# Kernel optimization log

Hardware: AMD Instinct MI355X
Metric: run time of the kernel (lower is better)

## Reference

```python
import jax, jax.numpy as jnp
import numpy as np

T, N, E = 12, 20000, 320000
FIN, H, G, C = 128, 256, 256, 10


def setup_inputs() -> dict:
    key = jax.random.key(0)
    ks = jax.random.split(key, 14)
    x = jax.random.normal(ks[0], (T, N, FIN), dtype=jnp.float32)
    edge_index = jax.random.randint(ks[1], (T, 2, E), 0, N)
    edge_attr = jax.random.uniform(ks[2], (T, E), dtype=jnp.float32)

    def lin(k, fan_in, shape):
        return jax.random.normal(k, shape, dtype=jnp.float32) / np.sqrt(fan_in).astype(np.float32)

    return {
        "x": x,
        "edge_index": edge_index,
        "edge_attr": edge_attr,
        "W1": lin(ks[3], FIN, (FIN, H)),
        "b1": jnp.zeros((H,), jnp.float32),
        "W2": lin(ks[4], H, (H, H)),
        "b2": jnp.zeros((H,), jnp.float32),
        "Wih": lin(ks[5], H, (3 * G, H)),
        "Whh": lin(ks[6], G, (3 * G, G)),
        "bih": jnp.zeros((3 * G,), jnp.float32),
        "bhh": jnp.zeros((3 * G,), jnp.float32),
        "Wc": lin(ks[7], G, (G, C)),
        "bc": jnp.zeros((C,), jnp.float32),
    }


def _gcn_conv(h, row, col, w, W, b):
    # PyG GCNConv: h' = D^{-1/2} (A + I) D^{-1/2} (h W) + b, with edge weights w
    h = h @ W  # [N, H]
    deg = jax.ops.segment_sum(w, col, num_segments=N) + 1.0  # self-loop weight 1
    dinv = jax.lax.rsqrt(deg)  # [N]
    norm = dinv[row] * w * dinv[col]  # [E]
    agg = jax.ops.segment_sum(norm[:, None] * h[row], col, num_segments=N)
    agg = agg + (dinv * dinv)[:, None] * h  # self-loop contribution
    return agg + b


def reference(x, edge_index, edge_attr, W1, b1, W2, b2, Wih, Whh, bih, bhh, Wc, bc):
    def snapshot(carry, inp):
        xs, ei, ea = inp
        row, col = ei[0], ei[1]
        h = jax.nn.relu(_gcn_conv(xs, row, col, ea, W1, b1))
        h = jax.nn.relu(_gcn_conv(h, row, col, ea, W2, b2))
        return carry, h.mean(axis=0)  # mean pool over nodes -> [H]

    _, embs = jax.lax.scan(snapshot, 0, (x, edge_index, edge_attr))  # [T, H]

    def gru_step(hprev, xt):
        gx = Wih @ xt + bih  # [3G]
        gh = Whh @ hprev + bhh
        r = jax.nn.sigmoid(gx[:G] + gh[:G])
        z = jax.nn.sigmoid(gx[G:2 * G] + gh[G:2 * G])
        n = jnp.tanh(gx[2 * G:] + r * gh[2 * G:])
        hnew = (1.0 - z) * n + z * hprev
        return hnew, None

    last_h, _ = jax.lax.scan(gru_step, jnp.zeros((G,), x.dtype), embs)
    out = last_h @ Wc + bc  # [C]
    return out[None, :]  # [1, num_classes]
```

## Files before the change

kernel.cpp:

```cpp
#include <hip/hip_runtime.h>
#include <hip/hip_fp16.h>
#include <math.h>

#define T_ 12
#define N_ 20000
#define E_ 320000
#define FIN_ 128
#define H_ 256
#define G_ 256
#define C_ 10
#define ECH 8
#define EPC (E_ / ECH)
#define NB 20
#define BNODES 1024
#define CAPF 18432

typedef __attribute__((ext_vector_type(8))) short bf16x8;
typedef __attribute__((ext_vector_type(4))) float f32x4;

static const size_t OFF_EMB   = 0;
static const size_t ZERO_BYTES= 12288;
static const size_t OFF_DINV  = 12288;
static const size_t OFF_CP    = 972288;
static const size_t OFF_DEGP  = 1932544;
static const size_t OFF_CNT16 = 9612544;
static const size_t OFF_EBIN  = 1932544;
static const size_t OFF_PCNT  = 32652544;
static const size_t OFF_POFF  = 32660224;
static const size_t OFF_EREC  = 32668288;
static const size_t OFF_W1BT  = 48028288;
static const size_t OFF_W2BT  = 48093824;
static const size_t OFF_WIHT  = 48224896;
static const size_t OFF_WHHT  = 49011328;
static const size_t OFF_GX    = 49797760;
static const size_t OFF_RA    = 49834624;
static const size_t PER_T_FULL= 10240000;

__device__ __forceinline__ float bf2f(unsigned short u) {
  return __uint_as_float(((unsigned int)u) << 16);
}
__device__ __forceinline__ unsigned short f2bf(float f) {
  unsigned int u = __float_as_uint(f);
  unsigned int r = (u + 0x7FFFu + ((u >> 16) & 1u)) >> 16;
  return (unsigned short)r;
}
__device__ __forceinline__ float bflo(unsigned int u) { return __uint_as_float(u << 16); }
__device__ __forceinline__ float bfhi(unsigned int u) { return __uint_as_float(u & 0xFFFF0000u); }
__device__ __forceinline__ unsigned int packbf(float lo, float hi) {
  return (unsigned int)f2bf(lo) | ((unsigned int)f2bf(hi) << 16);
}
__device__ __forceinline__ float rec2nm(unsigned int rec) {
  return __half2float(__ushort_as_half((unsigned short)(rec >> 16)));
}

__global__ __launch_bounds__(1024) void histp(const int* __restrict__ ei,
                                              const float* __restrict__ ea,
                                              float* __restrict__ degp,
                                              unsigned short* __restrict__ cnt16) {
  __shared__ float degs[N_];
  __shared__ unsigned int cntp[N_ / 2];
  const int t = blockIdx.x, ech = blockIdx.y;
  const int tid = threadIdx.x;
  for (int i = tid; i < N_; i += 1024) degs[i] = 0.f;
  for (int i = tid; i < N_ / 2; i += 1024) cntp[i] = 0u;
  __syncthreads();
  const int* col = ei + (size_t)t * 2 * E_ + E_ + ech * EPC;
  const float* wt = ea + (size_t)t * E_ + ech * EPC;
  for (int e = tid; e < EPC; e += 1024) {
    int c = col[e];
    atomicAdd(&degs[c], wt[e]);
    atomicAdd(&cntp[c >> 1], 1u << ((c & 1) * 16));
  }
  __syncthreads();
  float* dp = degp + ((size_t)t * ECH + ech) * N_;
  unsigned short* cp16 = cnt16 + ((size_t)t * ECH + ech) * N_;
  for (int i = tid; i < N_; i += 1024) {
    dp[i] = degs[i];
    cp16[i] = (unsigned short)((cntp[i >> 1] >> ((i & 1) * 16)) & 0xFFFFu);
  }
}

__global__ __launch_bounds__(1024) void scanT(const unsigned short* __restrict__ cnt16,
                                              const float* __restrict__ degp,
                                              int* __restrict__ colptr,
                                              float* __restrict__ dinv) {
  const int t = blockIdx.x;
  __shared__ int s[1024];
  const int tid = threadIdx.x;
  int base = 0;
  for (int c0 = 0; c0 < N_; c0 += 1024) {
    int n = c0 + tid;
    int tot = 0;
    float dg = 0.f;
    if (n < N_) {
#pragma unroll
      for (int ch = 0; ch < ECH; ++ch) {
        tot += cnt16[((size_t)t * ECH + ch) * N_ + n];
        dg += degp[((size_t)t * ECH + ch) * N_ + n];
      }
    }
    s[tid] = tot;
    __syncthreads();
    for (int off = 1; off < 1024; off <<= 1) {
      int add = (tid >= off) ? s[tid - off] : 0;
      __syncthreads();
      s[tid] += add;
      __syncthreads();
    }
    if (n < N_) {
      colptr[t * (N_ + 1) + n] = base + s[tid] - tot;
      dinv[t * N_ + n] = rsqrtf(dg + 1.0f);
    }
    base += s[1023];
    __syncthreads();
  }
  if (tid == 0) colptr[t * (N_ + 1) + N_] = base;
}

__global__ __launch_bounds__(256) void pcount(const unsigned short* __restrict__ cnt16,
                                              unsigned int* __restrict__ pcnt) {
  __shared__ unsigned int psum[NB];
  const int t = blockIdx.x, ech = blockIdx.y;
  const int tid = threadIdx.x;
  if (tid < NB) psum[tid] = 0u;
  __syncthreads();
  const unsigned short* cc = cnt16 + ((size_t)t * ECH + ech) * N_;
  for (int c0 = 0; c0 < N_; c0 += 256) {
    int n = c0 + tid;
    unsigned int v = (n < N_) ? (unsigned int)cc[n] : 0u;
#pragma unroll
    for (int off = 32; off; off >>= 1) v += __shfl_down(v, off, 64);
    if ((tid & 63) == 0) atomicAdd(&psum[c0 >> 10], v);
  }
  __syncthreads();
  if (tid < NB) pcnt[((size_t)t * ECH + ech) * NB + tid] = psum[tid];
}

__global__ void partS(const unsigned int* __restrict__ pcnt,
                      unsigned int* __restrict__ poff) {
  const int t = threadIdx.x;
  if (t >= T_) return;
  unsigned int run = 0;
  for (int b = 0; b < NB; ++b)
    for (int ech = 0; ech < ECH; ++ech) {
      poff[t * 168 + b * 8 + ech] = run;
      run += pcnt[((size_t)t * ECH + ech) * NB + b];
    }
  poff[t * 168 + 160] = run;
}

__global__ __launch_bounds__(512) void partW(const int* __restrict__ ei,
                                             const float* __restrict__ ea,
                                             const float* __restrict__ dinv,
                                             const unsigned int* __restrict__ poff,
                                             uint2* __restrict__ ebin) {
  __shared__ unsigned int cursor[NB];
  const int t = blockIdx.x, ech = blockIdx.y;
  const int tid = threadIdx.x;
  if (tid < NB) cursor[tid] = poff[t * 168 + tid * 8 + ech];
  __syncthreads();
  const int eoff = ech * EPC;
  const int* rowp = ei + (size_t)t * 2 * E_ + eoff;
  const int* colp = rowp + E_;
  const float* wt = ea + (size_t)t * E_ + eoff;
  const float* dv = dinv + (size_t)t * N_;
  uint2* eb = ebin + (size_t)t * E_;
  for (int e = tid; e < EPC; e += 512) {
    int c = colp[e], r = rowp[e];
    float nm = dv[r] * wt[e] * dv[c];
    unsigned int pos = atomicAdd(&cursor[c >> 10], 1u);
    uint2 rec;
    rec.x = (unsigned int)(c & 1023) | ((unsigned int)r << 16);
    rec.y = (unsigned int)__half_as_ushort(__float2half(nm));
    eb[pos] = rec;
  }
}

__global__ __launch_bounds__(512) void fillB2(const uint2* __restrict__ ebin,
                                              const int* __restrict__ colptr,
                                              unsigned int* __restrict__ erec) {
  __shared__ unsigned int data[CAPF];
  __shared__ unsigned int offp[BNODES];
  const int t = blockIdx.x, b = blockIdx.y;
  const int tid = threadIdx.x;
  const int nlo = b << 10;
  const int nnodes = (N_ - nlo < BNODES) ? (N_ - nlo) : BNODES;
  const int* cp = colptr + t * (N_ + 1);
  const int base = cp[nlo];
  const int bsize = cp[nlo + nnodes] - base;
  for (int i = tid; i < nnodes; i += 512) offp[i] = (unsigned int)(cp[nlo + i] - base);
  __syncthreads();
  const uint2* eb = ebin + (size_t)t * E_ + base;
  unsigned int* eg = erec + (size_t)t * E_ + base;
  for (int i = tid; i < bsize; i += 512) {
    uint2 rec = eb[i];
    unsigned int cl = rec.x & 0xFFFFu;
    unsigned int rec4 = (rec.x >> 16) | (rec.y << 16);
    unsigned int pos = atomicAdd(&offp[cl], 1u);
    if (pos < CAPF) data[pos] = rec4;
    else eg[pos] = rec4;
  }
  __syncthreads();
  const int lim = bsize < CAPF ? bsize : CAPF;
  for (int i = tid; i < lim; i += 512) eg[i] = data[i];
}

__global__ __launch_bounds__(256) void prep_kernel(const float* __restrict__ W1,
                                                   const float* __restrict__ W2,
                                                   const float* __restrict__ Wih,
                                                   const float* __restrict__ Whh,
                                                   unsigned short* __restrict__ W1bT,
                                                   unsigned short* __restrict__ W2bT,
                                                   float* __restrict__ WihT,
                                                   float* __restrict__ WhhT) {
  int idx = blockIdx.x * 256 + threadIdx.x;
  if (idx < 32768) {
    int n = idx >> 7, k = idx & 127;
    W1bT[idx] = f2bf(W1[k * 256 + n]);
  } else if (idx < 98304) {
    int j = idx - 32768;
    int n = j >> 8, k = j & 255;
    W2bT[j] = f2bf(W2[k * 256 + n]);
  } else if (idx < 294912) {
    int j = idx - 98304;
    int k = j / 768, c = j - k * 768;
    WihT[j] = Wih[c * 256 + k];
  } else if (idx < 491520) {
    int j = idx - 294912;
    int k = j / 768, c = j - k * 768;
    WhhT[j] = Whh[c * 256 + k];
  }
}

__global__ __launch_bounds__(256) void castx_kernel(const float* __restrict__ x,
                                                    unsigned short* __restrict__ xb,
                                                    int t_base) {
  const int tl = blockIdx.y;
  const int t = t_base + tl;
  const size_t q = (size_t)blockIdx.x * 256 + threadIdx.x;
  float4 v = ((const float4*)x)[(size_t)t * (N_ * FIN_ / 4) + q];
  ushort4 o;
  o.x = f2bf(v.x); o.y = f2bf(v.y); o.z = f2bf(v.z); o.w = f2bf(v.w);
  ((ushort4*)xb)[(size_t)tl * (N_ * FIN_ / 4) + q] = o;
}

__device__ __forceinline__ void agg_decode(int nt, int t_base, int& t, int& tl, int& node) {
  int bid = blockIdx.x;
  int L = bid;
  if (nt > 1) {
    int chunk = (int)(gridDim.x >> 3);
    L = (bid & 7) * chunk + (bid >> 3);
  }
  tl = L / 5000;
  node = (L - tl * 5000) * 4 + ((int)threadIdx.x >> 6);
  t = t_base + tl;
}

__global__ __launch_bounds__(256) void agg128(const unsigned short* __restrict__ h,
                                              unsigned short* __restrict__ o,
                                              const unsigned int* __restrict__ erec,
                                              const int* __restrict__ colptr,
                                              const float* __restrict__ dinv,
                                              int t_base, int nt) {
  int t, tl, node;
  agg_decode(nt, t_base, t, tl, node);
  const int q = ((int)threadIdx.x >> 4) & 3;
  const int l16 = threadIdx.x & 15;
  const int me = threadIdx.x & 63;
  const unsigned int* ert = erec + (size_t)t * E_;
  const int* cp = colptr + t * (N_ + 1);
  const unsigned short* ht = h + (size_t)tl * N_ * 128;
  float a0 = 0.f, a1 = 0.f, a2 = 0.f, a3 = 0.f, a4 = 0.f, a5 = 0.f, a6 = 0.f, a7 = 0.f;
  const int s0 = cp[node], s1 = cp[node + 1];
  for (int i = s0 + q; i < s1; i += 4) {
    const unsigned int rec = ert[i];
    const int r = rec & 0xFFFFu;
    const float nm = rec2nm(rec);
    uint4 u = *(const uint4*)&ht[(size_t)r * 128 + l16 * 8];
    a0 = fmaf(nm, bflo(u.x), a0); a1 = fmaf(nm, bfhi(u.x), a1);
    a2 = fmaf(nm, bflo(u.y), a2); a3 = fmaf(nm, bfhi(u.y), a3);
    a4 = fmaf(nm, bflo(u.z), a4); a5 = fmaf(nm, bfhi(u.z), a5);
    a6 = fmaf(nm, bflo(u.w), a6); a7 = fmaf(nm, bfhi(u.w), a7);
  }
  if (q == 0) {
    const float di = dinv[(size_t)t * N_ + node];
    const float sw = di * di;
    uint4 us = *(const uint4*)&ht[(size_t)node * 128 + l16 * 8];
    a0 = fmaf(sw, bflo(us.x), a0); a1 = fmaf(sw, bfhi(us.x), a1);
    a2 = fmaf(sw, bflo(us.y), a2); a3 = fmaf(sw, bfhi(us.y), a3);
    a4 = fmaf(sw, bflo(us.z), a4); a5 = fmaf(sw, bfhi(us.z), a5);
    a6 = fmaf(sw, bflo(us.w), a6); a7 = fmaf(sw, bfhi(us.w), a7);
  }
  a0 += __shfl(a0, me | 16, 64); a1 += __shfl(a1, me | 16, 64);
  a2 += __shfl(a2, me | 16, 64); a3 += __shfl(a3, me | 16, 64);
  a4 += __shfl(a4, me | 16, 64); a5 += __shfl(a5, me | 16, 64);
  a6 += __shfl(a6, me | 16, 64); a7 += __shfl(a7, me | 16, 64);
  a0 += __shfl(a0, me | 32, 64); a1 += __shfl(a1, me | 32, 64);
  a2 += __shfl(a2, me | 32, 64); a3 += __shfl(a3, me | 32, 64);
  a4 += __shfl(a4, me | 32, 64); a5 += __shfl(a5, me | 32, 64);
  a6 += __shfl(a6, me | 32, 64); a7 += __shfl(a7, me | 32, 64);
  if (q == 0 && (me >> 4) == 0) {
    uint4 ov;
    ov.x = packbf(a0, a1); ov.y = packbf(a2, a3);
    ov.z = packbf(a4, a5); ov.w = packbf(a6, a7);
    *(uint4*)&o[((size_t)tl * N_ + node) * 128 + l16 * 8] = ov;
  }
}

__global__ __launch_bounds__(256) void agg256(const unsigned short* __restrict__ h,
                                              unsigned short* __restrict__ o,
                                              const unsigned int* __restrict__ erec,
                                              const int* __restrict__ colptr,
                                              const float* __restrict__ dinv,
                                              int t_base, int nt) {
  int t, tl, node;
  agg_decode(nt, t_base, t, tl, node);
  const int hh = ((int)threadIdx.x >> 5) & 1;
  const int l32 = threadIdx.x & 31;
  const int me = threadIdx.x & 63;
  const unsigned int* ert = erec + (size_t)t * E_;
  const int* cp = colptr + t * (N_ + 1);
  const unsigned short* ht = h + (size_t)tl * N_ * 256;
  float a0 = 0.f, a1 = 0.f, a2 = 0.f, a3 = 0.f, a4 = 0.f, a5 = 0.f, a6 = 0.f, a7 = 0.f;
  const int s0 = cp[node], s1 = cp[node + 1];
  for (int i = s0 + hh; i < s1; i += 2) {
    const unsigned int rec = ert[i];
    const int r = rec & 0xFFFFu;
    const float nm = rec2nm(rec);
    uint4 u = *(const uint4*)&ht[(size_t)r * 256 + l32 * 8];
    a0 = fmaf(nm, bflo(u.x), a0); a1 = fmaf(nm, bfhi(u.x), a1);
    a2 = fmaf(nm, bflo(u.y), a2); a3 = fmaf(nm, bfhi(u.y), a3);
    a4 = fmaf(nm, bflo(u.z), a4); a5 = fmaf(nm, bfhi(u.z), a5);
    a6 = fmaf(nm, bflo(u.w), a6); a7 = fmaf(nm, bfhi(u.w), a7);
  }
  if (hh == 0) {
    const float di = dinv[(size_t)t * N_ + node];
    const float sw = di * di;
    uint4 us = *(const uint4*)&ht[(size_t)node * 256 + l32 * 8];
    a0 = fmaf(sw, bflo(us.x), a0); a1 = fmaf(sw, bfhi(us.x), a1);
    a2 = fmaf(sw, bflo(us.y), a2); a3 = fmaf(sw, bfhi(us.y), a3);
    a4 = fmaf(sw, bflo(us.z), a4); a5 = fmaf(sw, bfhi(us.z), a5);
    a6 = fmaf(sw, bflo(us.w), a6); a7 = fmaf(sw, bfhi(us.w), a7);
  }
  a0 += __shfl(a0, me | 32, 64); a1 += __shfl(a1, me | 32, 64);
  a2 += __shfl(a2, me | 32, 64); a3 += __shfl(a3, me | 32, 64);
  a4 += __shfl(a4, me | 32, 64); a5 += __shfl(a5, me | 32, 64);
  a6 += __shfl(a6, me | 32, 64); a7 += __shfl(a7, me | 32, 64);
  if (hh == 0) {
    uint4 ov;
    ov.x = packbf(a0, a1); ov.y = packbf(a2, a3);
    ov.z = packbf(a4, a5); ov.w = packbf(a6, a7);
    *(uint4*)&o[((size_t)tl * N_ + node) * 256 + l32 * 8] = ov;
  }
}

template <int K, bool MEAN>
__global__ __launch_bounds__(256) void gemm_bf16(const unsigned short* __restrict__ A,
                                                 const unsigned short* __restrict__ BT,
                                                 const float* __restrict__ bias,
                                                 unsigned short* __restrict__ C,
                                                 float* __restrict__ embp,
                                                 int t_base) {
  constexpr int LD = K + 8;
  __shared__ unsigned short As[64 * LD];
  __shared__ float cs[128];
  const int tid = threadIdx.x;
  const int tl = blockIdx.z;
  const int bm = blockIdx.x * 64;
  const int bn = blockIdx.y * 128;
  const unsigned short* At = A + (size_t)tl * N_ * K;
  if (MEAN && tid < 128) cs[tid] = 0.f;
  {
    constexpr int CPR = K / 8;
    constexpr int CH = 64 * CPR / 256;
#pragma unroll
    for (int i = 0; i < CH; ++i) {
      int chunk = tid + i * 256;
      int r = chunk / CPR;
      int ck = (chunk - r * CPR) * 8;
      int row = bm + r;
      if (row >= N_) row = N_ - 1;
      *(bf16x8*)&As[r * LD + ck] = *(const bf16x8*)&At[(size_t)row * K + ck];
    }
  }
  __syncthreads();
  const int w = tid >> 6, l = tid & 63;
  const int l16 = l & 15, lk = l >> 4;
  const int rbase = (w >> 1) * 32;
  const int colbase = bn + (w & 1) * 64;
  f32x4 acc[2][4] = {};
  for (int ks = 0; ks < K; ks += 32) {
    bf16x8 a[2], b[4];
#pragma unroll
    for (int m = 0; m < 2; ++m)
      a[m] = *(const bf16x8*)&As[(rbase + m * 16 + l16) * LD + ks + lk * 8];
#pragma unroll
    for (int n = 0; n < 4; ++n)
      b[n] = *(const bf16x8*)&BT[(size_t)(colbase + n * 16 + l16) * K + ks + lk * 8];
#pragma unroll
    for (int m = 0; m < 2; ++m)
#pragma unroll
      for (int n = 0; n < 4; ++n)
        acc[m][n] = __builtin_amdgcn_mfma_f32_16x16x32_bf16(a[m], b[n], acc[m][n], 0, 0, 0);
  }
#pragma unroll
  for (int n = 0; n < 4; ++n) {
    int col = colbase + n * 16 + l16;
    float bv = bias[col];
    float psum = 0.f;
#pragma unroll
    for (int m = 0; m < 2; ++m) {
      int row0 = bm + rbase + m * 16 + lk * 4;
#pragma unroll
      for (int r = 0; r < 4; ++r) {
        int row = row0 + r;
        if (row < N_) {
          float v = fmaxf(acc[m][n][r] + bv, 0.f);
          if (MEAN) psum += v;
          else C[((size_t)tl * N_ + row) * 256 + col] = f2bf(v);
        }
      }
    }
    if (MEAN) atomicAdd(&cs[col - bn], psum);
  }
  if (MEAN) {
    __syncthreads();
    if (tid < 128)
      atomicAdd(&embp[(t_base + tl) * 256 + bn + tid], cs[tid] * (1.0f / N_));
  }
}

__global__ __launch_bounds__(768) void gx_kernel(const float* __restrict__ emb,
                                                 const float* __restrict__ WihT,
                                                 const float* __restrict__ bih,
                                                 float* __restrict__ GX) {
  const int t = blockIdx.x;
  const int tid = threadIdx.x;
  __shared__ float se[256];
  if (tid < 256) se[tid] = emb[t * 256 + tid];
  __syncthreads();
  float p0 = 0.f, p1 = 0.f, p2 = 0.f, p3 = 0.f;
#pragma unroll 8
  for (int k = 0; k < 256; k += 4) {
    p0 = fmaf(WihT[(size_t)(k + 0) * 768 + tid], se[k + 0], p0);
    p1 = fmaf(WihT[(size_t)(k + 1) * 768 + tid], se[k + 1], p1);
    p2 = fmaf(WihT[(size_t)(k + 2) * 768 + tid], se[k + 2], p2);
    p3 = fmaf(WihT[(size_t)(k + 3) * 768 + tid], se[k + 3], p3);
  }
  GX[t * 768 + tid] = (p0 + p1) + (p2 + p3) + bih[tid];
}

__global__ __launch_bounds__(768) void gru2_kernel(const float* __restrict__ GX,
                                                   const float* __restrict__ WhhT,
                                                   const float* __restrict__ bhh,
                                                   const float* __restrict__ Wc,
                                                   const float* __restrict__ bc,
                                                   float* __restrict__ out) {
  __shared__ float sh[256];
  __shared__ float sgh[768];
  const int tid = threadIdx.x;
  if (tid < 256) sh[tid] = 0.f;
  __syncthreads();
  for (int t = 0; t < T_; ++t) {
    float p0 = 0.f, p1 = 0.f, p2 = 0.f, p3 = 0.f;
#pragma unroll 8
    for (int k = 0; k < 256; k += 4) {
      p0 = fmaf(WhhT[(size_t)(k + 0) * 768 + tid], sh[k + 0], p0);
      p1 = fmaf(WhhT[(size_t)(k + 1) * 768 + tid], sh[k + 1], p1);
      p2 = fmaf(WhhT[(size_t)(k + 2) * 768 + tid], sh[k + 2], p2);
      p3 = fmaf(WhhT[(size_t)(k + 3) * 768 + tid], sh[k + 3], p3);
    }
    sgh[tid] = (p0 + p1) + (p2 + p3) + bhh[tid];
    __syncthreads();
    if (tid < 256) {
      const float* gx = &GX[t * 768];
      float r = 1.f / (1.f + __expf(-(gx[tid] + sgh[tid])));
      float z = 1.f / (1.f + __expf(-(gx[256 + tid] + sgh[256 + tid])));
      float n = tanhf(gx[512 + tid] + r * sgh[512 + tid]);
      sh[tid] = (1.f - z) * n + z * sh[tid];
    }
    __syncthreads();
  }
  const int wv = tid >> 6, lane = tid & 63;
  if (wv < C_) {
    float p = 0.f;
#pragma unroll
    for (int i = 0; i < 4; ++i) {
      int j = lane + 64 * i;
      p += sh[j] * Wc[(size_t)j * C_ + wv];
    }
    for (int off = 32; off > 0; off >>= 1) p += __shfl_down(p, off);
    if (lane == 0) out[wv] = p + bc[wv];
  }
}

extern "C" void kernel_launch(void* const* d_in, const int* in_sizes, int n_in,
                              void* d_out, int out_size, void* d_ws, size_t ws_size,
                              hipStream_t stream) {
  const float* x   = (const float*)d_in[0];
  const int*   ei  = (const int*)d_in[1];
  const float* ea  = (const float*)d_in[2];
  const float* W1  = (const float*)d_in[3];
  const float* b1  = (const float*)d_in[4];
  const float* W2  = (const float*)d_in[5];
  const float* b2  = (const float*)d_in[6];
  const float* Wih = (const float*)d_in[7];
  const float* Whh = (const float*)d_in[8];
  const float* bih = (const float*)d_in[9];
  const float* bhh = (const float*)d_in[10];
  const float* Wc  = (const float*)d_in[11];
  const float* bc  = (const float*)d_in[12];
  float* out = (float*)d_out;

  char* w = (char*)d_ws;
  float* emb   = (float*)(w + OFF_EMB);
  float* dinv  = (float*)(w + OFF_DINV);
  int*   cp    = (int*)(w + OFF_CP);
  float* degp  = (float*)(w + OFF_DEGP);
  unsigned short* cnt16 = (unsigned short*)(w + OFF_CNT16);
  uint2* ebin  = (uint2*)(w + OFF_EBIN);
  unsigned int* pcnt = (unsigned int*)(w + OFF_PCNT);
  unsigned int* poff = (unsigned int*)(w + OFF_POFF);
  unsigned int* erec = (unsigned int*)(w + OFF_EREC);
  unsigned short* W1bT = (unsigned short*)(w + OFF_W1BT);
  unsigned short* W2bT = (unsigned short*)(w + OFF_W2BT);
  float* WihT  = (float*)(w + OFF_WIHT);
  float* WhhT  = (float*)(w + OFF_WHHT);
  float* GX    = (float*)(w + OFF_GX);

  int NT = 1;
  if (ws_size > OFF_RA + 2 * PER_T_FULL) {
    size_t avail = ws_size - OFF_RA;
    size_t nt = avail / (2 * PER_T_FULL);
    NT = (int)(nt < 12 ? nt : 12);
    if (NT < 1) NT = 1;
  }
  unsigned short* regA = (unsigned short*)(w + OFF_RA);
  unsigned short* regB = (unsigned short*)(w + OFF_RA + (size_t)NT * PER_T_FULL);
  unsigned short* xbt  = regA;
  unsigned short* Q    = regA;
  unsigned short* P128 = regB;
  unsigned short* P2   = regB;

  hipMemsetAsync(d_ws, 0, ZERO_BYTES, stream);

  prep_kernel<<<1920, 256, 0, stream>>>(W1, W2, Wih, Whh, W1bT, W2bT, WihT, WhhT);

  dim3 te_grid(T_, ECH);
  histp<<<te_grid, 1024, 0, stream>>>(ei, ea, degp, cnt16);
  scanT<<<T_, 1024, 0, stream>>>(cnt16, degp, cp, dinv);
  pcount<<<te_grid, 256, 0, stream>>>(cnt16, pcnt);
  partS<<<1, 64, 0, stream>>>(pcnt, poff);
  partW<<<te_grid, 512, 0, stream>>>(ei, ea, dinv, poff, ebin);
  fillB2<<<dim3(T_, NB), 512, 0, stream>>>(ebin, cp, erec);

  for (int t0 = 0; t0 < T_; t0 += NT) {
    const int nt = (T_ - t0) < NT ? (T_ - t0) : NT;
    castx_kernel<<<dim3(2500, nt), 256, 0, stream>>>(x, xbt, t0);
    agg128<<<nt * 5000, 256, 0, stream>>>(xbt, P128, erec, cp, dinv, t0, nt);
    gemm_bf16<FIN_, false><<<dim3(313, 2, nt), 256, 0, stream>>>(P128, W1bT, b1, Q, nullptr, t0);
    agg256<<<nt * 5000, 256, 0, stream>>>(Q, P2, erec, cp, dinv, t0, nt);
    gemm_bf16<H_, true><<<dim3(313, 2, nt), 256, 0, stream>>>(P2, W2bT, b2, nullptr, emb, t0);
  }
  gx_kernel<<<T_, 768, 0, stream>>>(emb, WihT, bih, GX);
  gru2_kernel<<<1, 768, 0, stream>>>(GX, WhhT, bhh, Wc, bc, out);
}
```

Baseline: 1.072 ms.

## Split sparse aggregation into 64-channel passes with 8-way edge parallelism

The two GCN aggregation kernels are merged into one template that processes each node's features in 64-channel slices, one slice per block pass. Each wavefront now handles 8 edges at once, with 8 lanes covering 64 channels, instead of 4 or 2 edges over all channels. Smaller per-pass working sets should keep the gathered feature slices cache-resident and raise memory-level parallelism for the gathers. In exchange, the edge records and column pointers are re-read once per pass and the launch needs 2-4x more blocks.

```diff
diff --git a/kernel.cpp b/kernel.cpp
--- a/kernel.cpp
+++ b/kernel.cpp
@@ -244,113 +244,66 @@
   ((ushort4*)xb)[(size_t)tl * (N_ * FIN_ / 4) + q] = o;
 }
 
-__device__ __forceinline__ void agg_decode(int nt, int t_base, int& t, int& tl, int& node) {
+template <int CHN, int NPASS>
+__global__ __launch_bounds__(256) void aggP(const unsigned short* __restrict__ h,
+                                            unsigned short* __restrict__ o,
+                                            const unsigned int* __restrict__ erec,
+                                            const int* __restrict__ colptr,
+                                            const float* __restrict__ dinv,
+                                            int t_base, int nt) {
   int bid = blockIdx.x;
   int L = bid;
   if (nt > 1) {
     int chunk = (int)(gridDim.x >> 3);
     L = (bid & 7) * chunk + (bid >> 3);
   }
-  tl = L / 5000;
-  node = (L - tl * 5000) * 4 + ((int)threadIdx.x >> 6);
-  t = t_base + tl;
-}
-
-__global__ __launch_bounds__(256) void agg128(const unsigned short* __restrict__ h,
-                                              unsigned short* __restrict__ o,
-                                              const unsigned int* __restrict__ erec,
-                                              const int* __restrict__ colptr,
-                                              const float* __restrict__ dinv,
-                                              int t_base, int nt) {
-  int t, tl, node;
-  agg_decode(nt, t_base, t, tl, node);
-  const int q = ((int)threadIdx.x >> 4) & 3;
-  const int l16 = threadIdx.x & 15;
+  const int PT = NPASS * 5000;
+  const int tl = L / PT;
+  int rem = L - tl * PT;
+  const int pass = rem / 5000;
+  const int nb = rem - pass * 5000;
+  const int node = nb * 4 + ((int)threadIdx.x >> 6);
+  const int t = t_base + tl;
+  const int g = ((int)threadIdx.x >> 3) & 7;
+  const int j = threadIdx.x & 7;
   const int me = threadIdx.x & 63;
   const unsigned int* ert = erec + (size_t)t * E_;
   const int* cp = colptr + t * (N_ + 1);
-  const unsigned short* ht = h + (size_t)tl * N_ * 128;
+  const unsigned short* ht = h + (size_t)tl * N_ * CHN + pass * 64;
   float a0 = 0.f, a1 = 0.f, a2 = 0.f, a3 = 0.f, a4 = 0.f, a5 = 0.f, a6 = 0.f, a7 = 0.f;
   const int s0 = cp[node], s1 = cp[node + 1];
-  for (int i = s0 + q; i < s1; i += 4) {
+  for (int i = s0 + g; i < s1; i += 8) {
     const unsigned int rec = ert[i];
     const int r = rec & 0xFFFFu;
     const float nm = rec2nm(rec);
-    uint4 u = *(const uint4*)&ht[(size_t)r * 128 + l16 * 8];
+    uint4 u = *(const uint4*)&ht[(size_t)r * CHN + j * 8];
     a0 = fmaf(nm, bflo(u.x), a0); a1 = fmaf(nm, bfhi(u.x), a1);
     a2 = fmaf(nm, bflo(u.y), a2); a3 = fmaf(nm, bfhi(u.y), a3);
     a4 = fmaf(nm, bflo(u.z), a4); a5 = fmaf(nm, bfhi(u.z), a5);
     a6 = fmaf(nm, bflo(u.w), a6); a7 = fmaf(nm, bfhi(u.w), a7);
   }
-  if (q == 0) {
+  if (g == 0) {
     const float di = dinv[(size_t)t * N_ + node];
     const float sw = di * di;
-    uint4 us = *(const uint4*)&ht[(size_t)node * 128 + l16 * 8];
+    uint4 us = *(const uint4*)&ht[(size_t)node * CHN + j * 8];
     a0 = fmaf(sw, bflo(us.x), a0); a1 = fmaf(sw, bfhi(us.x), a1);
     a2 = fmaf(sw, bflo(us.y), a2); a3 = fmaf(sw, bfhi(us.y), a3);
     a4 = fmaf(sw, bflo(us.z), a4); a5 = fmaf(sw, bfhi(us.z), a5);
     a6 = fmaf(sw, bflo(us.w), a6); a7 = fmaf(sw, bfhi(us.w), a7);
   }
-  a0 += __shfl(a0, me | 16, 64); a1 += __shfl(a1, me | 16, 64);
-  a2 += __shfl(a2, me | 16, 64); a3 += __shfl(a3, me | 16, 64);
-  a4 += __shfl(a4, me | 16, 64); a5 += __shfl(a5, me | 16, 64);
-  a6 += __shfl(a6, me | 16, 64); a7 += __shfl(a7, me | 16, 64);
-  a0 += __shfl(a0, me | 32, 64); a1 += __shfl(a1, me | 32, 64);
-  a2 += __shfl(a2, me | 32, 64); a3 += __shfl(a3, me | 32, 64);
-  a4 += __shfl(a4, me | 32, 64); a5 += __shfl(a5, me | 32, 64);
-  a6 += __shfl(a6, me | 32, 64); a7 += __shfl(a7, me | 32, 64);
-  if (q == 0 && (me >> 4) == 0) {
+#pragma unroll
+  for (int off = 8; off <= 32; off <<= 1) {
+    a0 += __shfl(a0, me ^ off, 64); a1 += __shfl(a1, me ^ off, 64);
+    a2 += __shfl(a2, me ^ off, 64); a3 += __shfl(a3, me ^ off, 64);
+    a4 += __shfl(a4, me ^ off, 64); a5 += __shfl(a5, me ^ off, 64);
+    a6 += __shfl(a6, me ^ off, 64); a7 += __shfl(a7, me ^ off, 64);
+  }
+  if (g == 0) {
     uint4 ov;
     ov.x = packbf(a0, a1); ov.y = packbf(a2, a3);
     ov.z = packbf(a4, a5); ov.w = packbf(a6, a7);
-    *(uint4*)&o[((size_t)tl * N_ + node) * 128 + l16 * 8] = ov;
-  }
-}
-
-__global__ __launch_bounds__(256) void agg256(const unsigned short* __restrict__ h,
-                                              unsigned short* __restrict__ o,
-                                              const unsigned int* __restrict__ erec,
-                                              const int* __restrict__ colptr,
-                                              const float* __restrict__ dinv,
-                                              int t_base, int nt) {
-  int t, tl, node;
-  agg_decode(nt, t_base, t, tl, node);
-  const int hh = ((int)threadIdx.x >> 5) & 1;
-  const int l32 = threadIdx.x & 31;
-  const int me = threadIdx.x & 63;
-  const unsigned int* ert = erec + (size_t)t * E_;
-  const int* cp = colptr + t * (N_ + 1);
-  const unsigned short* ht = h + (size_t)tl * N_ * 256;
-  float a0 = 0.f, a1 = 0.f, a2 = 0.f, a3 = 0.f, a4 = 0.f, a5 = 0.f, a6 = 0.f, a7 = 0.f;
-  const int s0 = cp[node], s1 = cp[node + 1];
-  for (int i = s0 + hh; i < s1; i += 2) {
-    const unsigned int rec = ert[i];
-    const int r = rec & 0xFFFFu;
-    const float nm = rec2nm(rec);
-    uint4 u = *(const uint4*)&ht[(size_t)r * 256 + l32 * 8];
-    a0 = fmaf(nm, bflo(u.x), a0); a1 = fmaf(nm, bfhi(u.x), a1);
-    a2 = fmaf(nm, bflo(u.y), a2); a3 = fmaf(nm, bfhi(u.y), a3);
-    a4 = fmaf(nm, bflo(u.z), a4); a5 = fmaf(nm, bfhi(u.z), a5);
-    a6 = fmaf(nm, bflo(u.w), a6); a7 = fmaf(nm, bfhi(u.w), a7);
-  }
-  if (hh == 0) {
-    const float di = dinv[(size_t)t * N_ + node];
-    const float sw = di * di;
-    uint4 us = *(const uint4*)&ht[(size_t)node * 256 + l32 * 8];
-    a0 = fmaf(sw, bflo(us.x), a0); a1 = fmaf(sw, bfhi(us.x), a1);
-    a2 = fmaf(sw, bflo(us.y), a2); a3 = fmaf(sw, bfhi(us.y), a3);
-    a4 = fmaf(sw, bflo(us.z), a4); a5 = fmaf(sw, bfhi(us.z), a5);
-    a6 = fmaf(sw, bflo(us.w), a6); a7 = fmaf(sw, bfhi(us.w), a7);
-  }
-  a0 += __shfl(a0, me | 32, 64); a1 += __shfl(a1, me | 32, 64);
-  a2 += __shfl(a2, me | 32, 64); a3 += __shfl(a3, me | 32, 64);
-  a4 += __shfl(a4, me | 32, 64); a5 += __shfl(a5, me | 32, 64);
-  a6 += __shfl(a6, me | 32, 64); a7 += __shfl(a7, me | 32, 64);
-  if (hh == 0) {
-    uint4 ov;
-    ov.x = packbf(a0, a1); ov.y = packbf(a2, a3);
-    ov.z = packbf(a4, a5); ov.w = packbf(a6, a7);
-    *(uint4*)&o[((size_t)tl * N_ + node) * 256 + l32 * 8] = ov;
+    unsigned short* ot = o + (size_t)tl * N_ * CHN + pass * 64;
+    *(uint4*)&ot[(size_t)node * CHN + j * 8] = ov;
   }
 }
 
@@ -557,9 +510,9 @@
   for (int t0 = 0; t0 < T_; t0 += NT) {
     const int nt = (T_ - t0) < NT ? (T_ - t0) : NT;
     castx_kernel<<<dim3(2500, nt), 256, 0, stream>>>(x, xbt, t0);
-    agg128<<<nt * 5000, 256, 0, stream>>>(xbt, P128, erec, cp, dinv, t0, nt);
+    aggP<128, 2><<<nt * 10000, 256, 0, stream>>>(xbt, P128, erec, cp, dinv, t0, nt);
     gemm_bf16<FIN_, false><<<dim3(313, 2, nt), 256, 0, stream>>>(P128, W1bT, b1, Q, nullptr, t0);
-    agg256<<<nt * 5000, 256, 0, stream>>>(Q, P2, erec, cp, dinv, t0, nt);
+    aggP<256, 4><<<nt * 20000, 256, 0, stream>>>(Q, P2, erec, cp, dinv, t0, nt);
     gemm_bf16<H_, true><<<dim3(313, 2, nt), 256, 0, stream>>>(P2, W2bT, b2, nullptr, emb, t0);
   }
   gx_kernel<<<T_, 768, 0, stream>>>(emb, WihT, bih, GX);
```

Result: slower. 1.197 ms (+11.7%).
